# Optimization experiments

Hardware: AMD Instinct MI355X
Metric: run time of the kernel (lower is better)

The kernel has to match this reference:

```python
import jax, jax.numpy as jnp
import numpy as np

WEIGHT = 0.85            # module init kwarg
LOW_T, HIGH_T = 0.1, 0.2  # kornia.filters.canny defaults
EPS = 1e-6


def _conv(x, k, padding):
    return jax.lax.conv_general_dilated(x, k, (1, 1), padding,
                                        dimension_numbers=('NCHW', 'OIHW', 'NCHW'))


def _gauss_kernel5():
    # kornia gaussian kernel, size 5, sigma 1
    x = jnp.arange(5, dtype=jnp.float32) - 2.0
    g = jnp.exp(-0.5 * x * x)
    g = g / g.sum()
    return jnp.outer(g, g)[None, None]  # [1,1,5,5]


_SOBEL = jnp.stack([
    jnp.array([[-1., 0., 1.], [-2., 0., 2.], [-1., 0., 1.]], jnp.float32),
    jnp.array([[-1., -2., -1.], [0., 0., 0.], [1., 2., 1.]], jnp.float32),
])[:, None]  # [2,1,3,3] unnormalized sobel (kornia spatial_gradient, normalized=False)

# 8 NMS directions in kornia's ordering: quantized angle k*45deg -> neighbor offset (dr, dc)
_OFFS = [(0, 1), (-1, 1), (-1, 0), (-1, -1), (0, -1), (1, -1), (1, 0), (1, 1)]


def _nms_kernels():
    k = np.zeros((8, 1, 3, 3), np.float32)
    for i, (dr, dc) in enumerate(_OFFS):
        k[i, 0, 1, 1] = 1.0
        k[i, 0, 1 + dr, 1 + dc] = -1.0
    return jnp.asarray(k)


_ONES3 = jnp.ones((1, 1, 3, 3), jnp.float32)


def canny_edges(img):
    """kornia.filters.canny(img)[1]; img: [N,1,H,W] -> binary edges [N,1,H,W]."""
    blurred = _conv(jnp.pad(img, ((0, 0), (0, 0), (2, 2), (2, 2)), mode='reflect'),
                    _gauss_kernel5(), 'VALID')
    grad = _conv(jnp.pad(blurred, ((0, 0), (0, 0), (1, 1), (1, 1)), mode='edge'),
                 _SOBEL, 'VALID')  # [N,2,H,W]
    gx, gy = grad[:, 0:1], grad[:, 1:2]
    mag = jnp.sqrt(gx * gx + gy * gy + EPS)
    ang = jnp.round(jnp.rad2deg(jnp.arctan2(gy, gx)) / 45.0) * 45.0
    # non-maximum suppression: (center - neighbor) along quantized direction, zero pad
    nms = _conv(mag, _nms_kernels(), [(1, 1), (1, 1)])  # [N,8,H,W]
    pos_idx = jnp.mod(ang / 45.0, 8.0).astype(jnp.int32)
    neg_idx = jnp.mod(ang / 45.0 + 4.0, 8.0).astype(jnp.int32)
    pos = jnp.take_along_axis(nms, pos_idx, axis=1)
    neg = jnp.take_along_axis(nms, neg_idx, axis=1)
    mag = mag * (jnp.minimum(pos, neg) > 0.0)
    # double threshold: weak -> 0.5, strong -> 1.0
    edges = 0.5 * (mag > LOW_T) + 0.5 * (mag > HIGH_T)

    # hysteresis: promote weak pixels 8-connected to a strong pixel, to fixed point
    def _promote(e):
        weak = (e == 0.5).astype(jnp.float32)
        strong = (e == 1.0).astype(jnp.float32)
        neigh = (_conv(strong, _ONES3, [(1, 1), (1, 1)]) > 0.0).astype(jnp.float32)
        return neigh * weak + strong, weak

    def _cond(state):
        e, e_old = state
        return jnp.any(e != e_old)

    def _body(state):
        e, _ = state
        new, weak = _promote(e)
        return new + (new == 0.0) * weak * 0.5, e

    edges, _ = jax.lax.while_loop(_cond, _body, (edges, -jnp.ones_like(edges)))
    out, _ = _promote(edges)  # final binary map: unpromoted weak pixels -> 0
    return out


def _mse(a, b):
    return jnp.mean((a - b) ** 2)


def setup_inputs() -> dict:
    key = jax.random.key(0)
    k1, k2 = jax.random.split(key)
    shape = (16, 12, 1, 256, 256)  # [B, T, C, H, W]
    pred_y = jax.random.uniform(k1, shape, dtype=jnp.float32)
    batch_y = jax.random.uniform(k2, shape, dtype=jnp.float32)
    return {"pred_y": pred_y, "batch_y": batch_y}


def reference(pred_y, batch_y):
    B, T, C, H, W = pred_y.shape
    ep = canny_edges(pred_y.reshape(B * T, C, H, W)).reshape(B, T, 1, H, W)
    et = canny_edges(batch_y.reshape(B * T, C, H, W)).reshape(B, T, 1, H, W)
    return WEIGHT * _mse(pred_y, batch_y) + (1.0 - WEIGHT) * _mse(ep, et)
```

## Files before the change

### kernel.cpp

```cpp
#include <hip/hip_runtime.h>

#define NIMG 192
#define NPIX (256*256)
#define N_TOTAL (192*65536)
typedef unsigned long long u64;

__device__ __forceinline__ int refl(int i){ i = i < 0 ? -i : i; return i > 255 ? 510 - i : i; }

__device__ __forceinline__ float dpp_shr1(float src, float oldv) {
    return __int_as_float(__builtin_amdgcn_update_dpp(
        __float_as_int(oldv), __float_as_int(src), 0x138, 0xF, 0xF, false));
}
__device__ __forceinline__ float dpp_shl1(float src, float oldv) {
    return __int_as_float(__builtin_amdgcn_update_dpp(
        __float_as_int(oldv), __float_as_int(src), 0x130, 0xF, 0xF, false));
}
__device__ __forceinline__ float dpp_shr1z(float src) {
    return __int_as_float(__builtin_amdgcn_update_dpp(
        0, __float_as_int(src), 0x138, 0xF, 0xF, true));
}
__device__ __forceinline__ float dpp_shl1z(float src) {
    return __int_as_float(__builtin_amdgcn_update_dpp(
        0, __float_as_int(src), 0x130, 0xF, 0xF, true));
}

__global__ __launch_bounds__(256, 3) void k_edges(
    const float* __restrict__ pred, const float* __restrict__ batch,
    u64* __restrict__ masks, double* __restrict__ sse)
{
    const int wv = threadIdx.x >> 6, lane = threadIdx.x & 63;
    const int band = blockIdx.x * 4 + wv;
    const int iy   = blockIdx.y;
    const int R0 = band * 32, R1 = R0 + 31;
    const bool isPred = iy < NIMG;
    const float* img  = isPred ? pred  + (size_t)iy * NPIX : batch + (size_t)(iy - NIMG) * NPIX;
    const float* oimg = isPred ? batch + (size_t)iy * NPIX : pred  + (size_t)(iy - NIMG) * NPIX;
    u64* mout = masks + (size_t)iy * 2048;
    const int mlo  = isPred ? R0 : R0 + 16;
    const int mloF = isPred ? R0 + 4 : R0 + 16;
    const unsigned spanF = isPred ? 11u : 15u;

    const float W0 = 0.0544886850f, W1 = 0.2442013420f, W2 = 0.4026199469f;
    const float LO2 = 0.01f, HI2 = 0.04f, T1 = 0.41421356237f;

    float hwB[4], hwC[4], hwD[4], hwE[4], boP[4], boQ[4];
    float mgA[4], mgB[4], mgAL, mgAR, mgBL, mgBR, gxp[4], gyp[4];
    float4 cur;
    float acc = 0.f;
    const float4 *pi = nullptr, *po = nullptr;
    u64* mo = nullptr;

    auto HB = [&](const float4& c, float hb[4]) {
        float Lz = dpp_shr1(c.z, c.z), Lw = dpp_shr1(c.w, c.y);
        float Rx = dpp_shl1(c.x, c.z), Ry = dpp_shl1(c.y, c.y);
        hb[0] = W0*(Lz + c.z) + W1*(Lw + c.y)  + W2*c.x;
        hb[1] = W0*(Lw + c.w) + W1*(c.x + c.z) + W2*c.y;
        hb[2] = W0*(c.x + Rx) + W1*(c.y + c.w) + W2*c.z;
        hb[3] = W0*(c.y + Ry) + W1*(c.z + Rx)  + W2*c.w;
    };
    auto VB = [&](const float a[4], const float b_[4], const float c[4],
                  const float d[4], const float e[4], float o[4]) {
        #pragma unroll
        for (int k = 0; k < 4; ++k) o[k] = W0*(a[k]+e[k]) + W1*(b_[k]+d[k]) + W2*c[k];
    };
    auto SOB = [&](const float lo[4], const float mid[4], const float hi[4],
                   float gx[4], float gy[4], float mg[4], float& SL, float& SR) {
        float t[4], u[4];
        #pragma unroll
        for (int k = 0; k < 4; ++k) { t[k] = lo[k] + 2.f*mid[k] + hi[k]; u[k] = hi[k] - lo[k]; }
        float Lt = dpp_shr1(t[3], t[0]), Rt = dpp_shl1(t[0], t[3]);
        float Lu = dpp_shr1(u[3], u[0]), Ru = dpp_shl1(u[0], u[3]);
        gx[0] = t[1] - Lt; gx[1] = t[2] - t[0]; gx[2] = t[3] - t[1]; gx[3] = Rt - t[2];
        gy[0] = (Lu + u[1]) + 2.f*u[0];  gy[1] = (u[0] + u[2]) + 2.f*u[1];
        gy[2] = (u[1] + u[3]) + 2.f*u[2]; gy[3] = (u[2] + Ru) + 2.f*u[3];
        #pragma unroll
        for (int k = 0; k < 4; ++k) mg[k] = fmaf(gx[k], gx[k], fmaf(gy[k], gy[k], 1e-6f));
        SL = dpp_shr1z(mg[3]); SR = dpp_shl1z(mg[0]);
    };
    auto MSE4 = [&](const float4& a, const float4& o) {
        float dx = a.x - o.x, dy = a.y - o.y, dz = a.z - o.z, dw = a.w - o.w;
        acc += dx*dx + dy*dy + dz*dz + dw*dw;
    };

    auto donms = [&](const float mgC[4], const float CL, const float CR, u64* dst) {
        u64 wB[4], sB[4];
        #pragma unroll
        for (int k = 0; k < 4; ++k) {
            const float gxv = gxp[k], gyv = gyp[k];
            const float ax = fabsf(gxv), ay = fabsf(gyv);
            const bool horiz = (ay <= T1 * ax);
            const bool vert  = (ax <= T1 * ay);
            const bool d45 = (int)(__float_as_uint(gxv) ^ __float_as_uint(gyv)) >= 0;
            const float Ap = (k < 3) ? mgA[k+1] : mgAR, Am = (k > 0) ? mgA[k-1] : mgAL;
            const float Bp = (k < 3) ? mgB[k+1] : mgBR, Bm = (k > 0) ? mgB[k-1] : mgBL;
            const float Cp = (k < 3) ? mgC[k+1] : CR,   Cm = (k > 0) ? mgC[k-1] : CL;
            const float m1 = horiz ? Bp : (vert ? mgC[k] : (d45 ? Ap : Cp));
            const float m2 = horiz ? Bm : (vert ? mgA[k] : (d45 ? Cm : Am));
            const float M  = fmaxf(fmaxf(m1, m2), LO2);
            const float v  = mgB[k];
            wB[k] = __ballot(v > M);
            sB[k] = __ballot(v > fmaxf(M, HI2));
        }
        if (lane == 0) {
            ulonglong2 q;
            q.x = wB[0]; q.y = wB[1]; ((ulonglong2*)dst)[0] = q;
            q.x = wB[2]; q.y = wB[3]; ((ulonglong2*)dst)[1] = q;
            q.x = sB[0]; q.y = sB[1]; ((ulonglong2*)dst)[2] = q;
            q.x = sB[2]; q.y = sB[3]; ((ulonglong2*)dst)[3] = q;
        }
    };

    auto steprow = [&](const int b) {
        float4 nxt = *(const float4*)(img + (size_t)refl(b + 3) * 256 + (lane << 2));
        const int m = b - 1, r = b - 2;
        const bool doM = (b + 2 >= mlo) && (b + 2 <= mlo + 15);
        float4 oc;
        if (doM) oc = *(const float4*)(oimg + (size_t)(b + 2) * 256 + (lane << 2));
        float hb[4];
        HB(cur, hb);
        float t[4], u[4], blv[4];
        #pragma unroll
        for (int k = 0; k < 4; ++k) {
            blv[k] = W0*(hwB[k] + hb[k]) + W1*(hwC[k] + hwE[k]) + W2*hwD[k];
            float lo = (m == 0)   ? boQ[k] : boP[k];
            float hi = (m == 255) ? boQ[k] : blv[k];
            t[k] = lo + 2.f*boQ[k] + hi;
            u[k] = hi - lo;
        }
        float Lt = dpp_shr1(t[3], t[0]), Rt = dpp_shl1(t[0], t[3]);
        float Lu = dpp_shr1(u[3], u[0]), Ru = dpp_shl1(u[0], u[3]);
        float gx[4], gy[4], mgC[4];
        gx[0] = t[1] - Lt; gx[1] = t[2] - t[0]; gx[2] = t[3] - t[1]; gx[3] = Rt - t[2];
        gy[0] = (Lu + u[1]) + 2.f*u[0];  gy[1] = (u[0] + u[2]) + 2.f*u[1];
        gy[2] = (u[1] + u[3]) + 2.f*u[2]; gy[3] = (u[2] + Ru) + 2.f*u[3];
        #pragma unroll
        for (int k = 0; k < 4; ++k) mgC[k] = fmaf(gx[k], gx[k], fmaf(gy[k], gy[k], 1e-6f));
        if (m < 0 || m > 255) { mgC[0]=mgC[1]=mgC[2]=mgC[3]=0.f; }
        float CL = dpp_shr1z(mgC[3]), CR = dpp_shl1z(mgC[0]);
        if (r >= R0 && r <= R1) donms(mgC, CL, CR, mout + r * 8);
        if (doM) MSE4(cur, oc);
        #pragma unroll
        for (int k = 0; k < 4; ++k) {
            hwB[k]=hwC[k]; hwC[k]=hwD[k]; hwD[k]=hwE[k]; hwE[k]=hb[k];
            boP[k]=boQ[k]; boQ[k]=blv[k];
            mgA[k]=mgB[k]; mgB[k]=mgC[k];
            gxp[k]=gx[k];  gyp[k]=gy[k];
        }
        mgAL=mgBL; mgBL=CL; mgAR=mgBR; mgBR=CR;
        cur = nxt;
    };

    auto fastrow = [&](const int b) {
        float4 nxt = *pi; pi += 64;
        const bool doM = ((unsigned)(b + 2 - mloF) <= spanF);
        float4 oc;
        if (doM) oc = *po;
        po += 64;
        float hb[4];
        HB(cur, hb);
        float blv[4];
        #pragma unroll
        for (int k = 0; k < 4; ++k)
            blv[k] = W0*(hwB[k] + hb[k]) + W1*(hwC[k] + hwE[k]) + W2*hwD[k];
        float gx[4], gy[4], mgC[4], CL, CR;
        SOB(boP, boQ, blv, gx, gy, mgC, CL, CR);
        donms(mgC, CL, CR, mo); mo += 8;
        if (doM) MSE4(cur, oc);
        #pragma unroll
        for (int k = 0; k < 4; ++k) {
            hwB[k]=hwC[k]; hwC[k]=hwD[k]; hwD[k]=hwE[k]; hwE[k]=hb[k];
            boP[k]=boQ[k]; boQ[k]=blv[k];
            mgA[k]=mgB[k]; mgB[k]=mgC[k];
            gxp[k]=gx[k];  gyp[k]=gy[k];
        }
        mgAL=mgBL; mgBL=CL; mgAR=mgBR; mgBR=CR;
        cur = nxt;
    };

    int b;
    if (band == 0) {
        #pragma unroll
        for (int k = 0; k < 4; ++k) {
            hwB[k]=hwC[k]=hwD[k]=hwE[k]=0.f; boP[k]=boQ[k]=0.f;
            mgA[k]=mgB[k]=0.f; gxp[k]=gyp[k]=0.f;
        }
        mgAL=mgAR=mgBL=mgBR=0.f;
        b = -6;
        cur = *(const float4*)(img + (size_t)refl(b + 2) * 256 + (lane << 2));
        for (; b <= 1; ++b) steprow(b);
        pi = (const float4*)img + ((size_t)5 << 6) + lane;
    } else {
        auto ldr = [&](int r){ return *((const float4*)(img  + (size_t)r * 256) + lane); };
        auto ldo = [&](int r){ return *((const float4*)(oimg + (size_t)r * 256) + lane); };
        float4 c0 = ldr(R0 - 4), c1 = ldr(R0 - 3);
        float h0[4],h1[4],h2[4],h3[4],h4[4],h5[4],h6[4],h7[4];
        float bo0[4],bo1[4],bo2[4],bo3[4];
        HB(c0, h0); c0 = ldr(R0 - 2);
        HB(c1, h1); c1 = ldr(R0 - 1);
        HB(c0, h2); c0 = ldr(R0);
        HB(c1, h3); c1 = ldr(R0 + 1);
        if (isPred) { float4 o = ldo(R0);     MSE4(c0, o); }
        HB(c0, h4); c0 = ldr(R0 + 2);
        if (isPred) { float4 o = ldo(R0 + 1); MSE4(c1, o); }
        HB(c1, h5); c1 = ldr(R0 + 3);
        VB(h0, h1, h2, h3, h4, bo0);
        VB(h1, h2, h3, h4, h5, bo1);
        if (isPred) { float4 o = ldo(R0 + 2); MSE4(c0, o); }
        HB(c0, h6); c0 = ldr(R0 + 4);
        VB(h2, h3, h4, h5, h6, bo2);
        { float dgx[4], dgy[4]; SOB(bo0, bo1, bo2, dgx, dgy, mgA, mgAL, mgAR); }
        if (isPred) { float4 o = ldo(R0 + 3); MSE4(c1, o); }
        HB(c1, h7);
        VB(h3, h4, h5, h6, h7, bo3);
        SOB(bo1, bo2, bo3, gxp, gyp, mgB, mgBL, mgBR);
        #pragma unroll
        for (int k = 0; k < 4; ++k) {
            hwB[k]=h4[k]; hwC[k]=h5[k]; hwD[k]=h6[k]; hwE[k]=h7[k];
            boP[k]=bo2[k]; boQ[k]=bo3[k];
        }
        cur = c0;
        pi = (const float4*)img + ((size_t)(R0 + 5) << 6) + lane;
        b = R0 + 2;
    }
    po = (const float4*)oimg + ((size_t)(R0 + 4) << 6) + lane;
    mo = mout + (size_t)R0 * 8;

    const int quads = (band == 7) ? 6 : 8;
    for (int q = 0; q < quads; ++q) {
        fastrow(b); fastrow(b + 1); fastrow(b + 2); fastrow(b + 3); b += 4;
    }
    if (band == 7) {
        fastrow(b); fastrow(b + 1); fastrow(b + 2); b += 3;
        for (; b <= 257; ++b) steprow(b);
    }

    for (int off = 32; off; off >>= 1) acc += __shfl_down(acc, off);
    if (lane == 0)
        atomicAdd(&sse[(blockIdx.y * 2 + blockIdx.x) & 63], (double)acc);
}

__global__ __launch_bounds__(256) void k_hyst(const u64* __restrict__ masks,
                                              u64* __restrict__ cnt)
{
    const int pr = blockIdx.x;
    const u64* rp = masks + (size_t)pr * 2048 + (size_t)threadIdx.x * 8;
    const u64* rt = masks + (size_t)(pr + NIMG) * 2048 + (size_t)threadIdx.x * 8;
    const int r = threadIdx.x;
    __shared__ u64 hd[8][256];
    __shared__ int flg[2];
    __shared__ int wsum[4];
    ulonglong2 a0 = ((const ulonglong2*)rp)[0];
    ulonglong2 a1 = ((const ulonglong2*)rp)[1];
    ulonglong2 a2 = ((const ulonglong2*)rp)[2];
    ulonglong2 a3 = ((const ulonglong2*)rp)[3];
    ulonglong2 b0 = ((const ulonglong2*)rt)[0];
    ulonglong2 b1 = ((const ulonglong2*)rt)[1];
    ulonglong2 b2 = ((const ulonglong2*)rt)[2];
    ulonglong2 b3 = ((const ulonglong2*)rt)[3];
    u64 pw0=a0.x, pw1=a0.y, pw2=a1.x, pw3=a1.y;
    u64 ps0=a2.x, ps1=a2.y, ps2=a3.x, ps3=a3.y;
    u64 tw0=b0.x, tw1=b0.y, tw2=b1.x, tw3=b1.y;
    u64 ts0=b2.x, ts1=b2.y, ts2=b3.x, ts3=b3.y;
    if (r < 2) flg[r] = 0;
    const int up = r ? r - 1 : 0, dn = (r < 255) ? r + 1 : 255;
    for (int k = 0;; ++k) {
        u64 hp0 = ps0 | (ps3 << 1) | ps1;
        u64 hp1 = ps1 | ps0 | ps2;
        u64 hp2 = ps2 | ps1 | ps3;
        u64 hp3 = ps3 | ps2 | (ps0 >> 1);
        u64 ht0 = ts0 | (ts3 << 1) | ts1;
        u64 ht1 = ts1 | ts0 | ts2;
        u64 ht2 = ts2 | ts1 | ts3;
        u64 ht3 = ts3 | ts2 | (ts0 >> 1);
        hd[0][r]=hp0; hd[1][r]=hp1; hd[2][r]=hp2; hd[3][r]=hp3;
        hd[4][r]=ht0; hd[5][r]=ht1; hd[6][r]=ht2; hd[7][r]=ht3;
        if (r == 0) flg[(k + 1) & 1] = 0;
        __syncthreads();
        u64 n0 = ps0 | ((hp0 | hd[0][up] | hd[0][dn]) & pw0);
        u64 n1 = ps1 | ((hp1 | hd[1][up] | hd[1][dn]) & pw1);
        u64 n2 = ps2 | ((hp2 | hd[2][up] | hd[2][dn]) & pw2);
        u64 n3 = ps3 | ((hp3 | hd[3][up] | hd[3][dn]) & pw3);
        u64 m0 = ts0 | ((ht0 | hd[4][up] | hd[4][dn]) & tw0);
        u64 m1 = ts1 | ((ht1 | hd[5][up] | hd[5][dn]) & tw1);
        u64 m2 = ts2 | ((ht2 | hd[6][up] | hd[6][dn]) & tw2);
        u64 m3 = ts3 | ((ht3 | hd[7][up] | hd[7][dn]) & tw3);
        u64 chg = (n0^ps0)|(n1^ps1)|(n2^ps2)|(n3^ps3)|(m0^ts0)|(m1^ts1)|(m2^ts2)|(m3^ts3);
        ps0=n0; ps1=n1; ps2=n2; ps3=n3; ts0=m0; ts1=m1; ts2=m2; ts3=m3;
        if (chg) flg[k & 1] = 1;
        __syncthreads();
        if (!flg[k & 1]) break;
    }
    int c = __popcll(ps0^ts0) + __popcll(ps1^ts1) + __popcll(ps2^ts2) + __popcll(ps3^ts3);
    for (int off = 32; off; off >>= 1) c += __shfl_down(c, off);
    if ((threadIdx.x & 63) == 0) wsum[threadIdx.x >> 6] = c;
    __syncthreads();
    if (threadIdx.x == 0)
        atomicAdd(cnt, (u64)(wsum[0] + wsum[1] + wsum[2] + wsum[3]));
}

__global__ void k_final(const double* __restrict__ sse, const u64* __restrict__ cnt,
                        float* __restrict__ out)
{
    double s = 0.0;
    for (int i = 0; i < 64; ++i) s += sse[i];
    float mse1 = (float)(s / (double)N_TOTAL);
    float mse2 = (float)((double)(*cnt) / (double)N_TOTAL);
    out[0] = 0.85f * mse1 + (1.0f - 0.85f) * mse2;
}

extern "C" void kernel_launch(void* const* d_in, const int* in_sizes, int n_in,
                              void* d_out, int out_size, void* d_ws, size_t ws_size,
                              hipStream_t stream)
{
    const float* pred  = (const float*)d_in[0];
    const float* batch = (const float*)d_in[1];
    float* out = (float*)d_out;
    double* sse = (double*)d_ws;
    u64* cnt    = (u64*)((char*)d_ws + 512);
    u64* masks  = (u64*)((char*)d_ws + 1024);

    hipMemsetAsync(d_ws, 0, 1024, stream);
    dim3 g1(2, 384);
    k_edges<<<g1, 256, 0, stream>>>(pred, batch, masks, sse);
    k_hyst<<<192, 256, 0, stream>>>(masks, cnt);
    k_final<<<1, 1, 0, stream>>>(sse, cnt, out);
}
```

Measured before the change: 64.55 us.

## Process pred and batch images together per wave with 16-row bands

Each wave now runs the blur/Sobel/NMS pipeline for both the pred and batch image of a pair at once, so the MSE term reuses the already-loaded rows instead of issuing separate loads of the other image. Bands shrink from 32 to 16 rows, with the grid changed to 4x192, keeping the total wave count. The cost is doubled register state per wave, which may lower occupancy, and more halo rows recomputed per band.

New measurement: 97.19 us. 50.6% more time.

```diff
diff --git a/kernel.cpp b/kernel.cpp
--- a/kernel.cpp
+++ b/kernel.cpp
@@ -30,25 +30,21 @@
 {
     const int wv = threadIdx.x >> 6, lane = threadIdx.x & 63;
     const int band = blockIdx.x * 4 + wv;
-    const int iy   = blockIdx.y;
-    const int R0 = band * 32, R1 = R0 + 31;
-    const bool isPred = iy < NIMG;
-    const float* img  = isPred ? pred  + (size_t)iy * NPIX : batch + (size_t)(iy - NIMG) * NPIX;
-    const float* oimg = isPred ? batch + (size_t)iy * NPIX : pred  + (size_t)(iy - NIMG) * NPIX;
-    u64* mout = masks + (size_t)iy * 2048;
-    const int mlo  = isPred ? R0 : R0 + 16;
-    const int mloF = isPred ? R0 + 4 : R0 + 16;
-    const unsigned spanF = isPred ? 11u : 15u;
+    const int pair = blockIdx.y;
+    const int R0 = band * 16, R1 = R0 + 15;
+    const float* imgs[2] = { pred + (size_t)pair * NPIX, batch + (size_t)pair * NPIX };
+    u64* mk[2] = { masks + (size_t)pair * 2048, masks + (size_t)(pair + NIMG) * 2048 };
 
     const float W0 = 0.0544886850f, W1 = 0.2442013420f, W2 = 0.4026199469f;
     const float LO2 = 0.01f, HI2 = 0.04f, T1 = 0.41421356237f;
 
-    float hwB[4], hwC[4], hwD[4], hwE[4], boP[4], boQ[4];
-    float mgA[4], mgB[4], mgAL, mgAR, mgBL, mgBR, gxp[4], gyp[4];
-    float4 cur;
+    float hwB[2][4], hwC[2][4], hwD[2][4], hwE[2][4], boP[2][4], boQ[2][4];
+    float mgA[2][4], mgB[2][4], mgAL[2], mgAR[2], mgBL[2], mgBR[2];
+    float gxp[2][4], gyp[2][4];
+    float4 cur[2];
     float acc = 0.f;
-    const float4 *pi = nullptr, *po = nullptr;
-    u64* mo = nullptr;
+    const float4* pi[2] = { nullptr, nullptr };
+    u64* mo[2] = { nullptr, nullptr };
 
     auto HB = [&](const float4& c, float hb[4]) {
         float Lz = dpp_shr1(c.z, c.z), Lw = dpp_shr1(c.w, c.y);
@@ -82,22 +78,26 @@
         acc += dx*dx + dy*dy + dz*dz + dw*dw;
     };
 
-    auto donms = [&](const float mgC[4], const float CL, const float CR, u64* dst) {
+    auto donms = [&](const int im, const float mgC[4], const float CL, const float CR,
+                     u64* dst) {
         u64 wB[4], sB[4];
         #pragma unroll
         for (int k = 0; k < 4; ++k) {
-            const float gxv = gxp[k], gyv = gyp[k];
+            const float gxv = gxp[im][k], gyv = gyp[im][k];
             const float ax = fabsf(gxv), ay = fabsf(gyv);
             const bool horiz = (ay <= T1 * ax);
             const bool vert  = (ax <= T1 * ay);
             const bool d45 = (int)(__float_as_uint(gxv) ^ __float_as_uint(gyv)) >= 0;
-            const float Ap = (k < 3) ? mgA[k+1] : mgAR, Am = (k > 0) ? mgA[k-1] : mgAL;
-            const float Bp = (k < 3) ? mgB[k+1] : mgBR, Bm = (k > 0) ? mgB[k-1] : mgBL;
-            const float Cp = (k < 3) ? mgC[k+1] : CR,   Cm = (k > 0) ? mgC[k-1] : CL;
-            const float m1 = horiz ? Bp : (vert ? mgC[k] : (d45 ? Ap : Cp));
-            const float m2 = horiz ? Bm : (vert ? mgA[k] : (d45 ? Cm : Am));
+            const float Ap = (k < 3) ? mgA[im][k+1] : mgAR[im];
+            const float Am = (k > 0) ? mgA[im][k-1] : mgAL[im];
+            const float Bp = (k < 3) ? mgB[im][k+1] : mgBR[im];
+            const float Bm = (k > 0) ? mgB[im][k-1] : mgBL[im];
+            const float Cp = (k < 3) ? mgC[k+1] : CR;
+            const float Cm = (k > 0) ? mgC[k-1] : CL;
+            const float m1 = horiz ? Bp : (vert ? mgC[k]     : (d45 ? Ap : Cp));
+            const float m2 = horiz ? Bm : (vert ? mgA[im][k] : (d45 ? Cm : Am));
             const float M  = fmaxf(fmaxf(m1, m2), LO2);
-            const float v  = mgB[k];
+            const float v  = mgB[im][k];
             wB[k] = __ballot(v > M);
             sB[k] = __ballot(v > fmaxf(M, HI2));
         }
@@ -110,133 +110,141 @@
         }
     };
 
+    const int glo = (band == 0) ? 0 : 252;
     auto steprow = [&](const int b) {
-        float4 nxt = *(const float4*)(img + (size_t)refl(b + 3) * 256 + (lane << 2));
         const int m = b - 1, r = b - 2;
-        const bool doM = (b + 2 >= mlo) && (b + 2 <= mlo + 15);
-        float4 oc;
-        if (doM) oc = *(const float4*)(oimg + (size_t)(b + 2) * 256 + (lane << 2));
-        float hb[4];
-        HB(cur, hb);
-        float t[4], u[4], blv[4];
-        #pragma unroll
-        for (int k = 0; k < 4; ++k) {
-            blv[k] = W0*(hwB[k] + hb[k]) + W1*(hwC[k] + hwE[k]) + W2*hwD[k];
-            float lo = (m == 0)   ? boQ[k] : boP[k];
-            float hi = (m == 255) ? boQ[k] : blv[k];
-            t[k] = lo + 2.f*boQ[k] + hi;
-            u[k] = hi - lo;
-        }
-        float Lt = dpp_shr1(t[3], t[0]), Rt = dpp_shl1(t[0], t[3]);
-        float Lu = dpp_shr1(u[3], u[0]), Ru = dpp_shl1(u[0], u[3]);
-        float gx[4], gy[4], mgC[4];
-        gx[0] = t[1] - Lt; gx[1] = t[2] - t[0]; gx[2] = t[3] - t[1]; gx[3] = Rt - t[2];
-        gy[0] = (Lu + u[1]) + 2.f*u[0];  gy[1] = (u[0] + u[2]) + 2.f*u[1];
-        gy[2] = (u[1] + u[3]) + 2.f*u[2]; gy[3] = (u[2] + Ru) + 2.f*u[3];
-        #pragma unroll
-        for (int k = 0; k < 4; ++k) mgC[k] = fmaf(gx[k], gx[k], fmaf(gy[k], gy[k], 1e-6f));
-        if (m < 0 || m > 255) { mgC[0]=mgC[1]=mgC[2]=mgC[3]=0.f; }
-        float CL = dpp_shr1z(mgC[3]), CR = dpp_shl1z(mgC[0]);
-        if (r >= R0 && r <= R1) donms(mgC, CL, CR, mout + r * 8);
-        if (doM) MSE4(cur, oc);
-        #pragma unroll
-        for (int k = 0; k < 4; ++k) {
-            hwB[k]=hwC[k]; hwC[k]=hwD[k]; hwD[k]=hwE[k]; hwE[k]=hb[k];
-            boP[k]=boQ[k]; boQ[k]=blv[k];
-            mgA[k]=mgB[k]; mgB[k]=mgC[k];
-            gxp[k]=gx[k];  gyp[k]=gy[k];
-        }
-        mgAL=mgBL; mgBL=CL; mgAR=mgBR; mgBR=CR;
-        cur = nxt;
+        float4 nxt[2];
+        #pragma unroll
+        for (int im = 0; im < 2; ++im)
+            nxt[im] = *(const float4*)(imgs[im] + (size_t)refl(b + 3) * 256 + (lane << 2));
+        #pragma unroll
+        for (int im = 0; im < 2; ++im) {
+            float hb[4];
+            HB(cur[im], hb);
+            float t[4], u[4], blv[4];
+            #pragma unroll
+            for (int k = 0; k < 4; ++k) {
+                blv[k] = W0*(hwB[im][k] + hb[k]) + W1*(hwC[im][k] + hwE[im][k]) + W2*hwD[im][k];
+                float lo = (m == 0)   ? boQ[im][k] : boP[im][k];
+                float hi = (m == 255) ? boQ[im][k] : blv[k];
+                t[k] = lo + 2.f*boQ[im][k] + hi;
+                u[k] = hi - lo;
+            }
+            float Lt = dpp_shr1(t[3], t[0]), Rt = dpp_shl1(t[0], t[3]);
+            float Lu = dpp_shr1(u[3], u[0]), Ru = dpp_shl1(u[0], u[3]);
+            float gx[4], gy[4], mgC[4];
+            gx[0] = t[1] - Lt; gx[1] = t[2] - t[0]; gx[2] = t[3] - t[1]; gx[3] = Rt - t[2];
+            gy[0] = (Lu + u[1]) + 2.f*u[0];  gy[1] = (u[0] + u[2]) + 2.f*u[1];
+            gy[2] = (u[1] + u[3]) + 2.f*u[2]; gy[3] = (u[2] + Ru) + 2.f*u[3];
+            #pragma unroll
+            for (int k = 0; k < 4; ++k) mgC[k] = fmaf(gx[k], gx[k], fmaf(gy[k], gy[k], 1e-6f));
+            if (m < 0 || m > 255) { mgC[0]=mgC[1]=mgC[2]=mgC[3]=0.f; }
+            float CL = dpp_shr1z(mgC[3]), CR = dpp_shl1z(mgC[0]);
+            if (r >= R0 && r <= R1) donms(im, mgC, CL, CR, mk[im] + r * 8);
+            #pragma unroll
+            for (int k = 0; k < 4; ++k) {
+                hwB[im][k]=hwC[im][k]; hwC[im][k]=hwD[im][k]; hwD[im][k]=hwE[im][k]; hwE[im][k]=hb[k];
+                boP[im][k]=boQ[im][k]; boQ[im][k]=blv[k];
+                mgA[im][k]=mgB[im][k]; mgB[im][k]=mgC[k];
+                gxp[im][k]=gx[k];  gyp[im][k]=gy[k];
+            }
+            mgAL[im]=mgBL[im]; mgBL[im]=CL; mgAR[im]=mgBR[im]; mgBR[im]=CR;
+        }
+        if ((unsigned)(b + 2 - glo) <= 3u) MSE4(cur[0], cur[1]);
+        cur[0] = nxt[0]; cur[1] = nxt[1];
     };
 
     auto fastrow = [&](const int b) {
-        float4 nxt = *pi; pi += 64;
-        const bool doM = ((unsigned)(b + 2 - mloF) <= spanF);
-        float4 oc;
-        if (doM) oc = *po;
-        po += 64;
-        float hb[4];
-        HB(cur, hb);
-        float blv[4];
-        #pragma unroll
-        for (int k = 0; k < 4; ++k)
-            blv[k] = W0*(hwB[k] + hb[k]) + W1*(hwC[k] + hwE[k]) + W2*hwD[k];
-        float gx[4], gy[4], mgC[4], CL, CR;
-        SOB(boP, boQ, blv, gx, gy, mgC, CL, CR);
-        donms(mgC, CL, CR, mo); mo += 8;
-        if (doM) MSE4(cur, oc);
-        #pragma unroll
-        for (int k = 0; k < 4; ++k) {
-            hwB[k]=hwC[k]; hwC[k]=hwD[k]; hwD[k]=hwE[k]; hwE[k]=hb[k];
-            boP[k]=boQ[k]; boQ[k]=blv[k];
-            mgA[k]=mgB[k]; mgB[k]=mgC[k];
-            gxp[k]=gx[k];  gyp[k]=gy[k];
-        }
-        mgAL=mgBL; mgBL=CL; mgAR=mgBR; mgBR=CR;
-        cur = nxt;
+        float4 nxt0 = *pi[0]; pi[0] += 64;
+        float4 nxt1 = *pi[1]; pi[1] += 64;
+        #pragma unroll
+        for (int im = 0; im < 2; ++im) {
+            float hb[4];
+            HB(cur[im], hb);
+            float blv[4];
+            #pragma unroll
+            for (int k = 0; k < 4; ++k)
+                blv[k] = W0*(hwB[im][k] + hb[k]) + W1*(hwC[im][k] + hwE[im][k]) + W2*hwD[im][k];
+            float gx[4], gy[4], mgC[4], CL, CR;
+            SOB(boP[im], boQ[im], blv, gx, gy, mgC, CL, CR);
+            donms(im, mgC, CL, CR, mo[im]); mo[im] += 8;
+            #pragma unroll
+            for (int k = 0; k < 4; ++k) {
+                hwB[im][k]=hwC[im][k]; hwC[im][k]=hwD[im][k]; hwD[im][k]=hwE[im][k]; hwE[im][k]=hb[k];
+                boP[im][k]=boQ[im][k]; boQ[im][k]=blv[k];
+                mgA[im][k]=mgB[im][k]; mgB[im][k]=mgC[k];
+                gxp[im][k]=gx[k];  gyp[im][k]=gy[k];
+            }
+            mgAL[im]=mgBL[im]; mgBL[im]=CL; mgAR[im]=mgBR[im]; mgBR[im]=CR;
+        }
+        if (b <= R1 - 2) MSE4(cur[0], cur[1]);
+        cur[0] = nxt0; cur[1] = nxt1;
     };
 
     int b;
     if (band == 0) {
         #pragma unroll
-        for (int k = 0; k < 4; ++k) {
-            hwB[k]=hwC[k]=hwD[k]=hwE[k]=0.f; boP[k]=boQ[k]=0.f;
-            mgA[k]=mgB[k]=0.f; gxp[k]=gyp[k]=0.f;
-        }
-        mgAL=mgAR=mgBL=mgBR=0.f;
-        b = -6;
-        cur = *(const float4*)(img + (size_t)refl(b + 2) * 256 + (lane << 2));
-        for (; b <= 1; ++b) steprow(b);
-        pi = (const float4*)img + ((size_t)5 << 6) + lane;
+        for (int im = 0; im < 2; ++im) {
+            #pragma unroll
+            for (int k = 0; k < 4; ++k) {
+                hwB[im][k]=hwC[im][k]=hwD[im][k]=hwE[im][k]=0.f; boP[im][k]=boQ[im][k]=0.f;
+                mgA[im][k]=mgB[im][k]=0.f; gxp[im][k]=gyp[im][k]=0.f;
+            }
+            mgAL[im]=mgAR[im]=mgBL[im]=mgBR[im]=0.f;
+            cur[im] = *(const float4*)(imgs[im] + (size_t)refl(-4) * 256 + (lane << 2));
+        }
+        for (b = -6; b <= 1; ++b) steprow(b);
+        pi[0] = (const float4*)imgs[0] + ((size_t)5 << 6) + lane;
+        pi[1] = (const float4*)imgs[1] + ((size_t)5 << 6) + lane;
     } else {
-        auto ldr = [&](int r){ return *((const float4*)(img  + (size_t)r * 256) + lane); };
-        auto ldo = [&](int r){ return *((const float4*)(oimg + (size_t)r * 256) + lane); };
-        float4 c0 = ldr(R0 - 4), c1 = ldr(R0 - 3);
-        float h0[4],h1[4],h2[4],h3[4],h4[4],h5[4],h6[4],h7[4];
-        float bo0[4],bo1[4],bo2[4],bo3[4];
-        HB(c0, h0); c0 = ldr(R0 - 2);
-        HB(c1, h1); c1 = ldr(R0 - 1);
-        HB(c0, h2); c0 = ldr(R0);
-        HB(c1, h3); c1 = ldr(R0 + 1);
-        if (isPred) { float4 o = ldo(R0);     MSE4(c0, o); }
-        HB(c0, h4); c0 = ldr(R0 + 2);
-        if (isPred) { float4 o = ldo(R0 + 1); MSE4(c1, o); }
-        HB(c1, h5); c1 = ldr(R0 + 3);
-        VB(h0, h1, h2, h3, h4, bo0);
-        VB(h1, h2, h3, h4, h5, bo1);
-        if (isPred) { float4 o = ldo(R0 + 2); MSE4(c0, o); }
-        HB(c0, h6); c0 = ldr(R0 + 4);
-        VB(h2, h3, h4, h5, h6, bo2);
-        { float dgx[4], dgy[4]; SOB(bo0, bo1, bo2, dgx, dgy, mgA, mgAL, mgAR); }
-        if (isPred) { float4 o = ldo(R0 + 3); MSE4(c1, o); }
-        HB(c1, h7);
-        VB(h3, h4, h5, h6, h7, bo3);
-        SOB(bo1, bo2, bo3, gxp, gyp, mgB, mgBL, mgBR);
-        #pragma unroll
-        for (int k = 0; k < 4; ++k) {
-            hwB[k]=h4[k]; hwC[k]=h5[k]; hwD[k]=h6[k]; hwE[k]=h7[k];
-            boP[k]=bo2[k]; boQ[k]=bo3[k];
-        }
-        cur = c0;
-        pi = (const float4*)img + ((size_t)(R0 + 5) << 6) + lane;
+        #pragma unroll
+        for (int im = 0; im < 2; ++im) {
+            auto ldr = [&](int r){ return *((const float4*)(imgs[im] + (size_t)r * 256) + lane); };
+            float4 c0 = ldr(R0 - 4), c1 = ldr(R0 - 3);
+            float h0[4],h1[4],h2[4],h3[4],h4[4],h5[4],h6[4],h7[4];
+            float bo0[4],bo1[4],bo2[4],bo3[4];
+            HB(c0, h0); c0 = ldr(R0 - 2);
+            HB(c1, h1); c1 = ldr(R0 - 1);
+            HB(c0, h2); c0 = ldr(R0);
+            HB(c1, h3); c1 = ldr(R0 + 1);
+            HB(c0, h4); c0 = ldr(R0 + 2);
+            HB(c1, h5); c1 = ldr(R0 + 3);
+            VB(h0, h1, h2, h3, h4, bo0);
+            VB(h1, h2, h3, h4, h5, bo1);
+            HB(c0, h6); c0 = ldr(R0 + 4);
+            VB(h2, h3, h4, h5, h6, bo2);
+            { float dgx[4], dgy[4]; SOB(bo0, bo1, bo2, dgx, dgy, mgA[im], mgAL[im], mgAR[im]); }
+            HB(c1, h7);
+            VB(h3, h4, h5, h6, h7, bo3);
+            SOB(bo1, bo2, bo3, gxp[im], gyp[im], mgB[im], mgBL[im], mgBR[im]);
+            #pragma unroll
+            for (int k = 0; k < 4; ++k) {
+                hwB[im][k]=h4[k]; hwC[im][k]=h5[k]; hwD[im][k]=h6[k]; hwE[im][k]=h7[k];
+                boP[im][k]=bo2[k]; boQ[im][k]=bo3[k];
+            }
+            cur[im] = c0;
+            pi[im] = (const float4*)imgs[im] + ((size_t)(R0 + 5) << 6) + lane;
+        }
+        #pragma unroll
+        for (int rr = 0; rr < 4; ++rr) {
+            float4 a = *((const float4*)(imgs[0] + (size_t)(R0 + rr) * 256) + lane);
+            float4 o = *((const float4*)(imgs[1] + (size_t)(R0 + rr) * 256) + lane);
+            MSE4(a, o);
+        }
         b = R0 + 2;
     }
-    po = (const float4*)oimg + ((size_t)(R0 + 4) << 6) + lane;
-    mo = mout + (size_t)R0 * 8;
-
-    const int quads = (band == 7) ? 6 : 8;
-    for (int q = 0; q < quads; ++q) {
-        fastrow(b); fastrow(b + 1); fastrow(b + 2); fastrow(b + 3); b += 4;
-    }
-    if (band == 7) {
-        fastrow(b); fastrow(b + 1); fastrow(b + 2); b += 3;
+    mo[0] = mk[0] + (size_t)R0 * 8;
+    mo[1] = mk[1] + (size_t)R0 * 8;
+
+    const int nfast = (band == 15) ? 8 : 16;
+    for (int i = 0; i < nfast; ++i) { fastrow(b); ++b; }
+    if (band == 15) {
         for (; b <= 257; ++b) steprow(b);
     }
 
     for (int off = 32; off; off >>= 1) acc += __shfl_down(acc, off);
     if (lane == 0)
-        atomicAdd(&sse[(blockIdx.y * 2 + blockIdx.x) & 63], (double)acc);
+        atomicAdd(&sse[(blockIdx.y * 4 + blockIdx.x) & 63], (double)acc);
 }
 
 __global__ __launch_bounds__(256) void k_hyst(const u64* __restrict__ masks,
@@ -320,7 +328,7 @@
     u64* masks  = (u64*)((char*)d_ws + 1024);
 
     hipMemsetAsync(d_ws, 0, 1024, stream);
-    dim3 g1(2, 384);
+    dim3 g1(4, 192);
     k_edges<<<g1, 256, 0, stream>>>(pred, batch, masks, sse);
     k_hyst<<<192, 256, 0, stream>>>(masks, cnt);
     k_final<<<1, 1, 0, stream>>>(sse, cnt, out);
```
